# Performance work log

Measured on AMD Instinct MI355X. Metric: run time of the kernel, lower is better.

The kernel has to match this reference:

```python
import jax, jax.numpy as jnp
import numpy as np
import math

D = 2048            # fc_feat_size (hardcoded sqrt(2048) scale in source)
IMAGES = 20         # images_per_person
NEIGHBOR = 5        # neighbor_size (sliding window width)
T = IMAGES - NEIGHBOR + 1   # number of windows = 16
SCALE = 1.0 / math.sqrt(2048.0)


def _attention(x, Wq, bq, Wk, bk, Wv, bv):
    # x: [N, L, D] -> [N, L, D]; bmm-softmax-bmm as in source
    q = x @ Wq.T + bq
    k = x @ Wk.T + bk
    v = x @ Wv.T + bv
    dot = jnp.einsum('nld,nmd->nlm', q, k) * SCALE
    w = jax.nn.softmax(dot, axis=-1)
    return jnp.einsum('nlm,nmd->nld', w, v)


def _lstm_final(x, Wih, Whh, bih, bhh):
    # PyTorch-convention LSTM (gates i,f,g,o); x: [N, L, D] -> final hidden [N, H]
    N = x.shape[0]
    H = Whh.shape[1]
    xg = x @ Wih.T + (bih + bhh)   # [N, L, 4H] precompute input projections

    def step(carry, xt):
        h, c = carry
        gates = xt + h @ Whh.T
        i, f, g, o = jnp.split(gates, 4, axis=-1)
        c = jax.nn.sigmoid(f) * c + jax.nn.sigmoid(i) * jnp.tanh(g)
        h = jax.nn.sigmoid(o) * jnp.tanh(c)
        return (h, c), None

    init = (jnp.zeros((N, H), x.dtype), jnp.zeros((N, H), x.dtype))
    (h, _), _ = jax.lax.scan(step, init, jnp.swapaxes(xg, 0, 1))
    return h


def _layernorm(x, g, b, eps=1e-5):
    mu = jnp.mean(x, axis=-1, keepdims=True)
    var = jnp.var(x, axis=-1, keepdims=True)
    return (x - mu) * jax.lax.rsqrt(var + eps) * g + b


def setup_inputs() -> dict:
    key = jax.random.key(0)
    ks = iter(jax.random.split(key, 32))
    s = 0.02
    p = {}
    p['fc_feats'] = jax.random.normal(next(ks), (64, IMAGES, D), jnp.float32)
    for pre in ('nsa', 'sa'):
        for nm in ('Wq', 'Wk', 'Wv'):
            p[f'{pre}_{nm}'] = jax.random.normal(next(ks), (D, D), jnp.float32) * s
        for nm in ('bq', 'bk', 'bv'):
            p[f'{pre}_{nm}'] = jnp.zeros((D,), jnp.float32)
        p[f'{pre}_Wih'] = jax.random.normal(next(ks), (4 * D, D), jnp.float32) * s
        p[f'{pre}_Whh'] = jax.random.normal(next(ks), (4 * D, D), jnp.float32) * s
        p[f'{pre}_bih'] = jnp.zeros((4 * D,), jnp.float32)
        p[f'{pre}_bhh'] = jnp.zeros((4 * D,), jnp.float32)
    p['ln_g'] = jnp.ones((D,), jnp.float32)
    p['ln_b'] = jnp.zeros((D,), jnp.float32)
    return p


def reference(fc_feats,
              nsa_Wq, nsa_Wk, nsa_Wv, nsa_bq, nsa_bk, nsa_bv,
              nsa_Wih, nsa_Whh, nsa_bih, nsa_bhh,
              sa_Wq, sa_Wk, sa_Wv, sa_bq, sa_bk, sa_bv,
              sa_Wih, sa_Whh, sa_bih, sa_bhh,
              ln_g, ln_b):
    B = fc_feats.shape[0]
    # Sliding windows: window t covers images [t, t+NEIGHBOR) -> [B, T, W, D]
    idx = jnp.arange(T)[:, None] + jnp.arange(NEIGHBOR)[None, :]
    windows = fc_feats[:, idx]                       # [B, T, W, D]
    wflat = windows.reshape(B * T, NEIGHBOR, D)
    # NeighboringSelfAttention: attention within window + LSTM final state
    att = _attention(wflat, nsa_Wq, nsa_bq, nsa_Wk, nsa_bk, nsa_Wv, nsa_bv)
    nsa = _lstm_final(att, nsa_Wih, nsa_Whh, nsa_bih, nsa_bhh)  # [B*T, D]
    nsa_feats = nsa.reshape(B, T, D)
    new_nsa_feats = _layernorm(nsa_feats, ln_g, ln_b)
    # SelfAttention over the T window summaries + LSTM final state
    att2 = _attention(new_nsa_feats, sa_Wq, sa_bq, sa_Wk, sa_bk, sa_Wv, sa_bv)
    sa_feats = _lstm_final(att2, sa_Wih, sa_Whh, sa_bih, sa_bhh)  # [B, D]
    return (sa_feats, new_nsa_feats)
```

## Files before the change

### kernel.cpp

```cpp
#include <hip/hip_runtime.h>
#include <hip/hip_bf16.h>

typedef unsigned int  u32;
typedef unsigned short u16;

typedef __bf16 bf16x8 __attribute__((ext_vector_type(8)));
typedef float  f32x4  __attribute__((ext_vector_type(4)));

#define D2048 2048
#define SCALE 0.022097086912079612f

__device__ __forceinline__ u32 f2bfbits(float f) {
    u32 u = __float_as_uint(f);
    return (u + 0x7FFFu + ((u >> 16) & 1u)) >> 16;
}
__device__ __forceinline__ u32 pack2(float a, float b) {
    return f2bfbits(a) | (f2bfbits(b) << 16);
}
__device__ __forceinline__ float bf2f(u32 h) {
    return __uint_as_float(h << 16);
}
__device__ __forceinline__ void unpack8(uint4 v, float* f) {
    f[0] = bf2f(v.x & 0xFFFFu); f[1] = bf2f(v.x >> 16);
    f[2] = bf2f(v.y & 0xFFFFu); f[3] = bf2f(v.y >> 16);
    f[4] = bf2f(v.z & 0xFFFFu); f[5] = bf2f(v.z >> 16);
    f[6] = bf2f(v.w & 0xFFFFu); f[7] = bf2f(v.w >> 16);
}
__device__ __forceinline__ float sigmf(float x) { return 1.f / (1.f + __expf(-x)); }
__device__ __forceinline__ float tanhf_(float x) {
    x = fminf(15.f, fmaxf(-15.f, x));
    float e = __expf(2.f * x);
    return (e - 1.f) / (e + 1.f);
}

__device__ __forceinline__ void gload_lds16(const u16* g, u16* l) {
    __builtin_amdgcn_global_load_lds(
        (const __attribute__((address_space(1))) unsigned int*)g,
        (__attribute__((address_space(3))) unsigned int*)l,
        16, 0, 0);
}

struct CvtArgs {
    const float* src[8];
    u16*         dst[8];
    int          n4[8];
    int          nseg;
};
__global__ __launch_bounds__(256) void cvt_multi(CvtArgs a) {
    int stride = gridDim.x * 256;
    for (int s = 0; s < a.nseg; ++s) {
        const float4* S = reinterpret_cast<const float4*>(a.src[s]);
        uint2*        D = reinterpret_cast<uint2*>(a.dst[s]);
        int n4 = a.n4[s];
        for (int i = blockIdx.x * 256 + threadIdx.x; i < n4; i += stride) {
            float4 v = S[i];
            uint2 p;
            p.x = pack2(v.x, v.y);
            p.y = pack2(v.z, v.w);
            D[i] = p;
        }
    }
}

template <bool OUT_BF16>
__global__ __launch_bounds__(512, 2) void gemm256(const u16* __restrict__ A, int lda,
                                                  const u16* __restrict__ B,
                                                  void* __restrict__ C0,
                                                  int M, int N, int K) {
    __shared__ u16 Ab[2][16384];
    __shared__ u16 Bb[2][16384];

    const int tid  = threadIdx.x;
    const int lane = tid & 63;
    const int wid  = tid >> 6;
    const int wm   = wid >> 2;
    const int wn   = wid & 3;
    const int l15  = lane & 15, l4 = lane >> 4;
    const int rowBase = blockIdx.y * 256;
    const int colBase = blockIdx.x * 256;

    const int srow8 = lane >> 3;
    const int scw   = ((lane & 7) ^ srow8) * 8;
    const u16* gA = A + (size_t)(rowBase + wid * 8 + srow8) * lda + scw;
    const u16* gB = B + (size_t)(colBase + wid * 8 + srow8) * (size_t)K + scw;
    const int ldsW = wid * 512;

#define STAGE_A(buf, koff, q) \
    gload_lds16(gA + (size_t)((q) * 64) * lda + (koff), &Ab[buf][(q) * 4096 + ldsW])
#define STAGE_B(buf, koff, q) \
    gload_lds16(gB + (size_t)((q) * 64) * (size_t)K + (koff), &Bb[buf][(q) * 4096 + ldsW])

    f32x4 acc[8][4];
#pragma unroll
    for (int m = 0; m < 8; m++)
#pragma unroll
        for (int n = 0; n < 4; n++) acc[m][n] = f32x4{0.f, 0.f, 0.f, 0.f};

    const int nt = K >> 6;

#pragma unroll
    for (int q = 0; q < 4; ++q) { STAGE_A(0, 0, q); STAGE_B(0, 0, q); }

    const int swzA = (l15 & 7);

    for (int t = 0; t < nt; ++t) {
        const int cur = t & 1;
        const int nxt = cur ^ 1;
        const int kN  = (t + 1) << 6;
        const bool more = (t + 1 < nt);

        if (more) {
            STAGE_A(nxt, kN, 0);
            STAGE_A(nxt, kN, 1);
            asm volatile("s_waitcnt vmcnt(2)" ::: "memory");
        } else {
            asm volatile("s_waitcnt vmcnt(0)" ::: "memory");
        }
        __builtin_amdgcn_s_barrier();

        bf16x8 bfrag[4][2];
#pragma unroll
        for (int n = 0; n < 4; ++n)
#pragma unroll
            for (int kk = 0; kk < 2; ++kk)
                bfrag[n][kk] = *reinterpret_cast<const bf16x8*>(
                    &Bb[cur][(wn * 64 + n * 16 + l15) * 64 +
                             (((kk * 4 + l4) ^ swzA) * 8)]);

#pragma unroll
        for (int p = 0; p < 4; ++p) {
            bf16x8 afr[2][2];
#pragma unroll
            for (int mi = 0; mi < 2; ++mi)
#pragma unroll
                for (int kk = 0; kk < 2; ++kk)
                    afr[mi][kk] = *reinterpret_cast<const bf16x8*>(
                        &Ab[cur][(wm * 128 + (p * 2 + mi) * 16 + l15) * 64 +
                                 (((kk * 4 + l4) ^ swzA) * 8)]);
            if (more) {
                if (p == 0)      { STAGE_A(nxt, kN, 2); STAGE_A(nxt, kN, 3); }
                else if (p == 1) { STAGE_B(nxt, kN, 0); STAGE_B(nxt, kN, 1); }
                else if (p == 2) { STAGE_B(nxt, kN, 2); STAGE_B(nxt, kN, 3); }
            }
            __builtin_amdgcn_s_barrier();
            __builtin_amdgcn_sched_barrier(0);
            __builtin_amdgcn_s_setprio(1);
#pragma unroll
            for (int kk = 0; kk < 2; ++kk)
#pragma unroll
                for (int mi = 0; mi < 2; ++mi)
#pragma unroll
                    for (int n = 0; n < 4; ++n)
                        acc[p * 2 + mi][n] = __builtin_amdgcn_mfma_f32_16x16x32_bf16(
                            afr[mi][kk], bfrag[n][kk], acc[p * 2 + mi][n], 0, 0, 0);
            __builtin_amdgcn_s_setprio(0);
            __builtin_amdgcn_sched_barrier(0);
            __builtin_amdgcn_s_barrier();
        }
    }
#undef STAGE_A
#undef STAGE_B

#pragma unroll
    for (int m = 0; m < 8; ++m) {
        int row0 = rowBase + wm * 128 + m * 16 + l4 * 4;
#pragma unroll
        for (int n = 0; n < 4; ++n) {
            int col = colBase + wn * 64 + n * 16 + l15;
#pragma unroll
            for (int rr = 0; rr < 4; ++rr) {
                if (OUT_BF16)
                    ((u16*)C0)[(size_t)(row0 + rr) * N + col] = (u16)f2bfbits(acc[m][n][rr]);
                else
                    ((float*)C0)[(size_t)(row0 + rr) * N + col] = acc[m][n][rr];
            }
        }
    }
}

__global__ __launch_bounds__(256) void gemm_qkv(const u16* __restrict__ A,
                                                const u16* __restrict__ B0,
                                                const u16* __restrict__ B1,
                                                const u16* __restrict__ B2,
                                                const float* __restrict__ bias0,
                                                const float* __restrict__ bias1,
                                                const float* __restrict__ bias2,
                                                u16* __restrict__ Cout,
                                                size_t zCstride,
                                                int M, int N, int K) {
    __shared__ u16 Abuf[2][128 * 64];
    __shared__ u16 Bbuf[2][128 * 64];

    const int tid  = threadIdx.x;
    const int lane = tid & 63;
    const int wave = tid >> 6;
    const int wr   = (wave >> 1) * 64;
    const int wc   = (wave & 1) * 64;
    const int rowBase = blockIdx.y * 128;
    const int colBase = blockIdx.x * 128;
    const int l15 = lane & 15, l4 = lane >> 4;
    const int srow = lane >> 3;
    const int scol = (lane & 7) * 8;

    const int z = blockIdx.z;
    const u16* B      = (z == 0) ? B0 : ((z == 1) ? B1 : B2);
    const float* bias = (z == 0) ? bias0 : ((z == 1) ? bias1 : bias2);
    u16* C = Cout + (size_t)z * zCstride;

    const u16* ga = A + (size_t)(rowBase + wave * 32 + srow) * K + scol;
    const u16* gb = B + (size_t)(colBase + wave * 32 + srow) * K + scol;
    const int ldsOff = (wave * 32) * 64;

    f32x4 acc[4][4];
#pragma unroll
    for (int i = 0; i < 4; i++)
#pragma unroll
        for (int j = 0; j < 4; j++) acc[i][j] = f32x4{0.f, 0.f, 0.f, 0.f};

    const int nt = K >> 6;

#pragma unroll
    for (int i = 0; i < 4; ++i) {
        gload_lds16(ga + (size_t)(i * 8) * K, &Abuf[0][ldsOff + i * 8 * 64]);
        gload_lds16(gb + (size_t)(i * 8) * K, &Bbuf[0][ldsOff + i * 8 * 64]);
    }

    for (int t = 0; t < nt; ++t) {
        const int cur = t & 1;
        if (t + 1 < nt) {
            const int k1 = (t + 1) << 6;
#pragma unroll
            for (int i = 0; i < 4; ++i) {
                gload_lds16(ga + (size_t)(i * 8) * K + k1,
                            &Abuf[cur ^ 1][ldsOff + i * 8 * 64]);
                gload_lds16(gb + (size_t)(i * 8) * K + k1,
                            &Bbuf[cur ^ 1][ldsOff + i * 8 * 64]);
            }
            asm volatile("s_waitcnt vmcnt(8)" ::: "memory");
        } else {
            asm volatile("s_waitcnt vmcnt(0)" ::: "memory");
        }
        __builtin_amdgcn_s_barrier();
        __builtin_amdgcn_sched_barrier(0);
#pragma unroll
        for (int kk = 0; kk < 2; ++kk) {
            bf16x8 af[4], bfr[4];
#pragma unroll
            for (int i = 0; i < 4; i++) {
                af[i]  = *reinterpret_cast<const bf16x8*>(
                    &Abuf[cur][(wr + i * 16 + l15) * 64 + kk * 32 + l4 * 8]);
                bfr[i] = *reinterpret_cast<const bf16x8*>(
                    &Bbuf[cur][(wc + i * 16 + l15) * 64 + kk * 32 + l4 * 8]);
            }
#pragma unroll
            for (int i = 0; i < 4; i++)
#pragma unroll
                for (int j = 0; j < 4; j++)
                    acc[i][j] = __builtin_amdgcn_mfma_f32_16x16x32_bf16(af[i], bfr[j],
                                                                        acc[i][j], 0, 0, 0);
        }
        __builtin_amdgcn_sched_barrier(0);
        __builtin_amdgcn_s_barrier();
    }

#pragma unroll
    for (int i = 0; i < 4; i++) {
        int row0 = rowBase + wr + i * 16 + l4 * 4;
#pragma unroll
        for (int j = 0; j < 4; j++) {
            int col = colBase + wc + j * 16 + l15;
            float bv = bias[col];
#pragma unroll
            for (int rr = 0; rr < 4; rr++)
                C[(size_t)(row0 + rr) * N + col] = (u16)f2bfbits(acc[i][j][rr] + bv);
        }
    }
}

__global__ __launch_bounds__(256) void gemm128_bf(const u16* __restrict__ A,
                                                  const u16* __restrict__ B,
                                                  u16* __restrict__ C,
                                                  int M, int N, int K) {
    __shared__ u16 Abuf[2][128 * 64];
    __shared__ u16 Bbuf[2][128 * 64];

    const int tid  = threadIdx.x;
    const int lane = tid & 63;
    const int wave = tid >> 6;
    const int wr   = (wave >> 1) * 64;
    const int wc   = (wave & 1) * 64;
    const int rowBase = blockIdx.y * 128;
    const int colBase = blockIdx.x * 128;
    const int l15 = lane & 15, l4 = lane >> 4;
    const int srow = lane >> 3;
    const int scol = (lane & 7) * 8;

    const u16* ga = A + (size_t)(rowBase + wave * 32 + srow) * K + scol;
    const u16* gb = B + (size_t)(colBase + wave * 32 + srow) * K + scol;
    const int ldsOff = (wave * 32) * 64;

    f32x4 acc[4][4];
#pragma unroll
    for (int i = 0; i < 4; i++)
#pragma unroll
        for (int j = 0; j < 4; j++) acc[i][j] = f32x4{0.f, 0.f, 0.f, 0.f};

    const int nt = K >> 6;

#pragma unroll
    for (int i = 0; i < 4; ++i) {
        gload_lds16(ga + (size_t)(i * 8) * K, &Abuf[0][ldsOff + i * 8 * 64]);
        gload_lds16(gb + (size_t)(i * 8) * K, &Bbuf[0][ldsOff + i * 8 * 64]);
    }

    for (int t = 0; t < nt; ++t) {
        const int cur = t & 1;
        if (t + 1 < nt) {
            const int k1 = (t + 1) << 6;
#pragma unroll
            for (int i = 0; i < 4; ++i) {
                gload_lds16(ga + (size_t)(i * 8) * K + k1,
                            &Abuf[cur ^ 1][ldsOff + i * 8 * 64]);
                gload_lds16(gb + (size_t)(i * 8) * K + k1,
                            &Bbuf[cur ^ 1][ldsOff + i * 8 * 64]);
            }
            asm volatile("s_waitcnt vmcnt(8)" ::: "memory");
        } else {
            asm volatile("s_waitcnt vmcnt(0)" ::: "memory");
        }
        __builtin_amdgcn_s_barrier();
        __builtin_amdgcn_sched_barrier(0);
#pragma unroll
        for (int kk = 0; kk < 2; ++kk) {
            bf16x8 af[4], bfr[4];
#pragma unroll
            for (int i = 0; i < 4; i++) {
                af[i]  = *reinterpret_cast<const bf16x8*>(
                    &Abuf[cur][(wr + i * 16 + l15) * 64 + kk * 32 + l4 * 8]);
                bfr[i] = *reinterpret_cast<const bf16x8*>(
                    &Bbuf[cur][(wc + i * 16 + l15) * 64 + kk * 32 + l4 * 8]);
            }
#pragma unroll
            for (int i = 0; i < 4; i++)
#pragma unroll
                for (int j = 0; j < 4; j++)
                    acc[i][j] = __builtin_amdgcn_mfma_f32_16x16x32_bf16(af[i], bfr[j],
                                                                        acc[i][j], 0, 0, 0);
        }
        __builtin_amdgcn_sched_barrier(0);
        __builtin_amdgcn_s_barrier();
    }

#pragma unroll
    for (int i = 0; i < 4; i++) {
        int row0 = rowBase + wr + i * 16 + l4 * 4;
#pragma unroll
        for (int j = 0; j < 4; j++) {
            int col = colBase + wc + j * 16 + l15;
#pragma unroll
            for (int rr = 0; rr < 4; rr++)
                C[(size_t)(row0 + rr) * N + col] = (u16)f2bfbits(acc[i][j][rr]);
        }
    }
}

template <bool LAST>
__global__ __launch_bounds__(256) void gemm_gate128(
    const u16* __restrict__ A,
    const u16* __restrict__ B,
    const u16* __restrict__ xg,
    int xg_stride,
    const float* __restrict__ bih,
    const float* __restrict__ bhh,
    float* __restrict__ c,
    u16* __restrict__ hbf_out,
    float* __restrict__ hf,
    int K) {
    __shared__ u16 smem[32768];
    u16* Ab = smem;
    u16* Bb = smem + 16384;

    const int tid = threadIdx.x, lane = tid & 63, wave = tid >> 6;
    const int wr = (wave >> 1) * 64, wc = (wave & 1) * 64;
    const int l15 = lane & 15, l4 = lane >> 4;
    const int srow = lane >> 3, scol = (lane & 7) * 8;
    const int jBase = blockIdx.x * 32;
    const int rowBase = blockIdx.y * 128;

    const u16* ga = A + (size_t)(rowBase + wave * 32 + srow) * K + scol;
    const u16* gb[4];
#pragma unroll
    for (int i = 0; i < 4; ++i) {
        int lc = wave * 32 + i * 8 + srow;
        int br = jBase + (lc & 31) + (lc >> 5) * 2048;
        gb[i] = B + (size_t)br * K + scol;
    }
    const int ldsOff = (wave * 32) * 64;

    f32x4 acc[4][4];
#pragma unroll
    for (int i = 0; i < 4; i++)
#pragma unroll
        for (int j = 0; j < 4; j++) acc[i][j] = f32x4{0.f, 0.f, 0.f, 0.f};

    const int nt = K >> 6;
#pragma unroll
    for (int i = 0; i < 4; ++i) {
        gload_lds16(ga + (size_t)(i * 8) * K, &Ab[ldsOff + i * 8 * 64]);
        gload_lds16(gb[i], &Bb[ldsOff + i * 8 * 64]);
    }

    for (int t = 0; t < nt; ++t) {
        const int cur = (t & 1) * 8192;
        if (t + 1 < nt) {
            const int k1 = (t + 1) << 6;
            const int nxt = ((t + 1) & 1) * 8192;
#pragma unroll
            for (int i = 0; i < 4; ++i) {
                gload_lds16(ga + (size_t)(i * 8) * K + k1, &Ab[nxt + ldsOff + i * 8 * 64]);
                gload_lds16(gb[i] + k1, &Bb[nxt + ldsOff + i * 8 * 64]);
            }
            asm volatile("s_waitcnt vmcnt(8)" ::: "memory");
        } else {
            asm volatile("s_waitcnt vmcnt(0)" ::: "memory");
        }
        __builtin_amdgcn_s_barrier();
        __builtin_amdgcn_sched_barrier(0);
#pragma unroll
        for (int kk = 0; kk < 2; ++kk) {
            bf16x8 af[4], bfr[4];
#pragma unroll
            for (int i = 0; i < 4; i++) {
                af[i]  = *reinterpret_cast<const bf16x8*>(
                    &Ab[cur + (wr + i * 16 + l15) * 64 + kk * 32 + l4 * 8]);
                bfr[i] = *reinterpret_cast<const bf16x8*>(
                    &Bb[cur + (wc + i * 16 + l15) * 64 + kk * 32 + l4 * 8]);
            }
#pragma unroll
            for (int i = 0; i < 4; i++)
#pragma unroll
                for (int j = 0; j < 4; j++)
                    acc[i][j] = __builtin_amdgcn_mfma_f32_16x16x32_bf16(af[i], bfr[j],
                                                                        acc[i][j], 0, 0, 0);
        }
        __builtin_amdgcn_sched_barrier(0);
        __builtin_amdgcn_s_barrier();
    }

    float* Cs = (float*)smem;
#pragma unroll
    for (int i = 0; i < 4; i++)
#pragma unroll
        for (int j = 0; j < 4; j++)
#pragma unroll
            for (int rr = 0; rr < 4; rr++)
                Cs[(wr + i * 16 + l4 * 4 + rr) * 128 + (wc + j * 16 + l15)] =
                    acc[i][j][rr];
    __syncthreads();

    const int j  = tid & 31;
    const int rb = tid >> 5;
    const int gj = jBase + j;
    const float bi_ = bih[gj]        + bhh[gj];
    const float bf_ = bih[gj + 2048] + bhh[gj + 2048];
    const float bg_ = bih[gj + 4096] + bhh[gj + 4096];
    const float bo_ = bih[gj + 6144] + bhh[gj + 6144];
#pragma unroll
    for (int k = 0; k < 16; ++k) {
        int r = rb * 16 + k;
        int n = rowBase + r;
        const u16* xr = xg + (size_t)n * xg_stride;
        float gi = Cs[r * 128 + j]      + bf2f((u32)xr[gj])        + bi_;
        float gf = Cs[r * 128 + 32 + j] + bf2f((u32)xr[gj + 2048]) + bf_;
        float gg = Cs[r * 128 + 64 + j] + bf2f((u32)xr[gj + 4096]) + bg_;
        float go = Cs[r * 128 + 96 + j] + bf2f((u32)xr[gj + 6144]) + bo_;
        size_t idx = (size_t)n * 2048 + gj;
        float cc = c[idx];
        float cn = sigmf(gf) * cc + sigmf(gi) * tanhf_(gg);
        float hn = sigmf(go) * tanhf_(cn);
        c[idx] = cn;
        hbf_out[idx] = (u16)f2bfbits(hn);
        if (LAST) hf[idx] = hn;
    }
}

__global__ __launch_bounds__(256) void gemm_gate64v2(
    const u16* __restrict__ A,
    const u16* __restrict__ B,
    const u16* __restrict__ xg,
    int xg_stride,
    const float* __restrict__ bih,
    const float* __restrict__ bhh,
    float* __restrict__ c,
    u16* __restrict__ hbf_out,
    float* __restrict__ hf,
    int K) {
    __shared__ u16 smem[12288];
    u16* Ab = smem;
    u16* Bb = smem + 8192;

    const int tid = threadIdx.x, lane = tid & 63, wave = tid >> 6;
    const int l15 = lane & 15, l4 = lane >> 4;
    const int srow = lane >> 3, scol = (lane & 7) * 8;
    const int jb = blockIdx.x;

    const u16* ga = A + (size_t)(wave * 16 + srow) * K + scol;
    const u16* gb = B + (size_t)(jb * 8 + srow + wave * 2048) * K + scol;
    const int aOff = (wave * 16) * 64;
    const int bOff = (wave * 8) * 64;

    f32x4 acc0 = f32x4{0.f, 0.f, 0.f, 0.f};
    f32x4 acc1 = f32x4{0.f, 0.f, 0.f, 0.f};

    const int nt = K >> 6;
    gload_lds16(ga,                 &Ab[aOff]);
    gload_lds16(ga + (size_t)8 * K, &Ab[aOff + 512]);
    gload_lds16(gb,                 &Bb[bOff]);

    for (int t = 0; t < nt; ++t) {
        const int curA = (t & 1) * 4096;
        const int curB = (t & 1) * 2048;
        if (t + 1 < nt) {
            const int k1 = (t + 1) << 6;
            const int nxA = ((t + 1) & 1) * 4096;
            const int nxB = ((t + 1) & 1) * 2048;
            gload_lds16(ga + k1,                 &Ab[nxA + aOff]);
            gload_lds16(ga + (size_t)8 * K + k1, &Ab[nxA + aOff + 512]);
            gload_lds16(gb + k1,                 &Bb[nxB + bOff]);
            asm volatile("s_waitcnt vmcnt(3)" ::: "memory");
        } else {
            asm volatile("s_waitcnt vmcnt(0)" ::: "memory");
        }
        __builtin_amdgcn_s_barrier();
        __builtin_amdgcn_sched_barrier(0);
#pragma unroll
        for (int kk = 0; kk < 2; ++kk) {
            bf16x8 af = *reinterpret_cast<const bf16x8*>(
                &Ab[curA + (wave * 16 + l15) * 64 + kk * 32 + l4 * 8]);
            bf16x8 b0 = *reinterpret_cast<const bf16x8*>(
                &Bb[curB + (l15) * 64 + kk * 32 + l4 * 8]);
            bf16x8 b1 = *reinterpret_cast<const bf16x8*>(
                &Bb[curB + (16 + l15) * 64 + kk * 32 + l4 * 8]);
            acc0 = __builtin_amdgcn_mfma_f32_16x16x32_bf16(af, b0, acc0, 0, 0, 0);
            acc1 = __builtin_amdgcn_mfma_f32_16x16x32_bf16(af, b1, acc1, 0, 0, 0);
        }
        __builtin_amdgcn_sched_barrier(0);
        __builtin_amdgcn_s_barrier();
    }

    float* Cs = (float*)smem;
    {
        int row0 = wave * 16 + l4 * 4;
#pragma unroll
        for (int rr = 0; rr < 4; ++rr) {
            Cs[(row0 + rr) * 32 + l15]      = acc0[rr];
            Cs[(row0 + rr) * 32 + 16 + l15] = acc1[rr];
        }
    }
    __syncthreads();

    const int j  = tid & 7;
    const int gj = jb * 8 + j;
    const float bi_ = bih[gj]        + bhh[gj];
    const float bf_ = bih[gj + 2048] + bhh[gj + 2048];
    const float bg_ = bih[gj + 4096] + bhh[gj + 4096];
    const float bo_ = bih[gj + 6144] + bhh[gj + 6144];
#pragma unroll
    for (int k = 0; k < 2; ++k) {
        int row = (tid >> 3) + k * 32;
        const u16* xr = xg + (size_t)row * xg_stride;
        float gi = Cs[row * 32 + j]      + bf2f((u32)xr[gj])        + bi_;
        float gf = Cs[row * 32 + 8 + j]  + bf2f((u32)xr[gj + 2048]) + bf_;
        float gg = Cs[row * 32 + 16 + j] + bf2f((u32)xr[gj + 4096]) + bg_;
        float go = Cs[row * 32 + 24 + j] + bf2f((u32)xr[gj + 6144]) + bo_;
        size_t idx = (size_t)row * 2048 + gj;
        float cc = c[idx];
        float cn = sigmf(gf) * cc + sigmf(gi) * tanhf_(gg);
        float hn = sigmf(go) * tanhf_(cn);
        c[idx] = cn;
        hbf_out[idx] = (u16)f2bfbits(hn);
        if (hf) hf[idx] = hn;
    }
}

__global__ __launch_bounds__(256) void lstm_gate0(const u16* __restrict__ xg,
                                                  int xg_stride,
                                                  const float* __restrict__ bih,
                                                  const float* __restrict__ bhh,
                                                  float* __restrict__ c,
                                                  u16* __restrict__ hbf,
                                                  int rows) {
    int idx = blockIdx.x * 256 + threadIdx.x;
    int total = rows * 512;
    if (idx >= total) return;
    int n  = idx >> 9;
    int j4 = (idx & 511) * 4;

    const u16* xr = xg + (size_t)n * xg_stride + j4;
    float4 gi, gg, go;
    {
        uint2 ri = *reinterpret_cast<const uint2*>(xr);
        uint2 rg = *reinterpret_cast<const uint2*>(xr + 4096);
        uint2 ro = *reinterpret_cast<const uint2*>(xr + 6144);
        gi = {bf2f(ri.x & 0xFFFFu), bf2f(ri.x >> 16), bf2f(ri.y & 0xFFFFu), bf2f(ri.y >> 16)};
        gg = {bf2f(rg.x & 0xFFFFu), bf2f(rg.x >> 16), bf2f(rg.y & 0xFFFFu), bf2f(rg.y >> 16)};
        go = {bf2f(ro.x & 0xFFFFu), bf2f(ro.x >> 16), bf2f(ro.y & 0xFFFFu), bf2f(ro.y >> 16)};
    }
    float4 bi1 = *reinterpret_cast<const float4*>(bih + j4);
    float4 bg1 = *reinterpret_cast<const float4*>(bih + 4096 + j4);
    float4 bo1 = *reinterpret_cast<const float4*>(bih + 6144 + j4);
    float4 bi2 = *reinterpret_cast<const float4*>(bhh + j4);
    float4 bg2 = *reinterpret_cast<const float4*>(bhh + 4096 + j4);
    float4 bo2 = *reinterpret_cast<const float4*>(bhh + 6144 + j4);

    gi.x += bi1.x + bi2.x; gi.y += bi1.y + bi2.y; gi.z += bi1.z + bi2.z; gi.w += bi1.w + bi2.w;
    gg.x += bg1.x + bg2.x; gg.y += bg1.y + bg2.y; gg.z += bg1.z + bg2.z; gg.w += bg1.w + bg2.w;
    go.x += bo1.x + bo2.x; go.y += bo1.y + bo2.y; go.z += bo1.z + bo2.z; go.w += bo1.w + bo2.w;

    float cx = sigmf(gi.x) * tanhf_(gg.x);
    float cy = sigmf(gi.y) * tanhf_(gg.y);
    float cz = sigmf(gi.z) * tanhf_(gg.z);
    float cw = sigmf(gi.w) * tanhf_(gg.w);
    float hx = sigmf(go.x) * tanhf_(cx);
    float hy = sigmf(go.y) * tanhf_(cy);
    float hz = sigmf(go.z) * tanhf_(cz);
    float hw_ = sigmf(go.w) * tanhf_(cw);

    float4 co = {cx, cy, cz, cw};
    *reinterpret_cast<float4*>(c + (size_t)n * 2048 + j4) = co;
    uint2 hp;
    hp.x = pack2(hx, hy);
    hp.y = pack2(hz, hw_);
    *reinterpret_cast<uint2*>(hbf + (size_t)n * 2048 + j4) = hp;
}

__global__ __launch_bounds__(256) void attn_win5(const u16* __restrict__ q0,
                                                 const u16* __restrict__ k0,
                                                 const u16* __restrict__ v0,
                                                 u16* __restrict__ att) {
    int n = blockIdx.x;
    int b = n >> 4, t = n & 15;
    int tid = threadIdx.x, lane = tid & 63, wave = tid >> 6;
    int d0 = tid * 8;
    size_t base = (size_t)(b * 20 + t) * D2048;

    float qv[5][8];
#pragma unroll
    for (int i = 0; i < 5; i++) {
        uint4 v = *reinterpret_cast<const uint4*>(q0 + base + (size_t)i * D2048 + d0);
        unpack8(v, qv[i]);
    }
    float part[25];
#pragma unroll
    for (int p = 0; p < 25; p++) part[p] = 0.f;
#pragma unroll
    for (int m = 0; m < 5; m++) {
        float kv[8];
        uint4 v = *reinterpret_cast<const uint4*>(k0 + base + (size_t)m * D2048 + d0);
        unpack8(v, kv);
#pragma unroll
        for (int l = 0; l < 5; l++)
#pragma unroll
            for (int j = 0; j < 8; j++) part[l * 5 + m] += qv[l][j] * kv[j];
    }
#pragma unroll
    for (int p = 0; p < 25; p++) {
        float s = part[p];
#pragma unroll
        for (int msk = 32; msk; msk >>= 1) s += __shfl_xor(s, msk, 64);
        part[p] = s;
    }
    __shared__ float wred[4][25];
    __shared__ float wmat[25];
    if (lane == 0) {
#pragma unroll
        for (int p = 0; p < 25; p++) wred[wave][p] = part[p];
    }
    __syncthreads();
    if (tid < 5) {
        int l = tid;
        float dv[5], mx = -1e30f;
#pragma unroll
        for (int m = 0; m < 5; m++) {
            dv[m] = (wred[0][l * 5 + m] + wred[1][l * 5 + m] + wred[2][l * 5 + m] +
                     wred[3][l * 5 + m]) * SCALE;
            mx = fmaxf(mx, dv[m]);
        }
        float ssum = 0.f;
#pragma unroll
        for (int m = 0; m < 5; m++) { dv[m] = __expf(dv[m] - mx); ssum += dv[m]; }
        float inv = 1.f / ssum;
#pragma unroll
        for (int m = 0; m < 5; m++) wmat[l * 5 + m] = dv[m] * inv;
    }
    __syncthreads();

    float oacc[5][8];
#pragma unroll
    for (int l = 0; l < 5; l++)
#pragma unroll
        for (int j = 0; j < 8; j++) oacc[l][j] = 0.f;
#pragma unroll
    for (int m = 0; m < 5; m++) {
        float vv[8];
        uint4 v = *reinterpret_cast<const uint4*>(v0 + base + (size_t)m * D2048 + d0);
        unpack8(v, vv);
#pragma unroll
        for (int l = 0; l < 5; l++) {
            float w = wmat[l * 5 + m];
#pragma unroll
            for (int j = 0; j < 8; j++) oacc[l][j] += w * vv[j];
        }
    }
#pragma unroll
    for (int l = 0; l < 5; l++) {
        uint4 p;
        p.x = pack2(oacc[l][0], oacc[l][1]);
        p.y = pack2(oacc[l][2], oacc[l][3]);
        p.z = pack2(oacc[l][4], oacc[l][5]);
        p.w = pack2(oacc[l][6], oacc[l][7]);
        *reinterpret_cast<uint4*>(att + (size_t)(n * 5 + l) * D2048 + d0) = p;
    }
}

__global__ __launch_bounds__(256) void attn_seq16(const u16* __restrict__ q2,
                                                  const u16* __restrict__ k2,
                                                  const u16* __restrict__ v2,
                                                  u16* __restrict__ att2) {
    int r = blockIdx.x;
    int b = r >> 4;
    int tid = threadIdx.x, lane = tid & 63, wave = tid >> 6;
    int d0 = tid * 8;
    size_t kbase = (size_t)b * 16 * D2048;

    float qv[8];
    {
        uint4 v = *reinterpret_cast<const uint4*>(q2 + (size_t)r * D2048 + d0);
        unpack8(v, qv);
    }
    float part[16];
#pragma unroll
    for (int m = 0; m < 16; m++) part[m] = 0.f;
#pragma unroll
    for (int m = 0; m < 16; m++) {
        float kv[8];
        uint4 v = *reinterpret_cast<const uint4*>(k2 + kbase + (size_t)m * D2048 + d0);
        unpack8(v, kv);
#pragma unroll
        for (int j = 0; j < 8; j++) part[m] += qv[j] * kv[j];
    }
#pragma unroll
    for (int m = 0; m < 16; m++) {
        float s = part[m];
#pragma unroll
        for (int msk = 32; msk; msk >>= 1) s += __shfl_xor(s, msk, 64);
        part[m] = s;
    }
    __shared__ float wred[4][16];
    __shared__ float wmat[16];
    if (lane == 0) {
#pragma unroll
        for (int m = 0; m < 16; m++) wred[wave][m] = part[m];
    }
    __syncthreads();
    if (tid == 0) {
        float dv[16], mx = -1e30f;
#pragma unroll
        for (int m = 0; m < 16; m++) {
            dv[m] = (wred[0][m] + wred[1][m] + wred[2][m] + wred[3][m]) * SCALE;
            mx = fmaxf(mx, dv[m]);
        }
        float ssum = 0.f;
#pragma unroll
        for (int m = 0; m < 16; m++) { dv[m] = __expf(dv[m] - mx); ssum += dv[m]; }
        float inv = 1.f / ssum;
#pragma unroll
        for (int m = 0; m < 16; m++) wmat[m] = dv[m] * inv;
    }
    __syncthreads();

    float oacc[8];
#pragma unroll
    for (int j = 0; j < 8; j++) oacc[j] = 0.f;
#pragma unroll
    for (int m = 0; m < 16; m++) {
        float vv[8];
        uint4 v = *reinterpret_cast<const uint4*>(v2 + kbase + (size_t)m * D2048 + d0);
        unpack8(v, vv);
        float w = wmat[m];
#pragma unroll
        for (int j = 0; j < 8; j++) oacc[j] += w * vv[j];
    }
    uint4 p;
    p.x = pack2(oacc[0], oacc[1]);
    p.y = pack2(oacc[2], oacc[3]);
    p.z = pack2(oacc[4], oacc[5]);
    p.w = pack2(oacc[6], oacc[7]);
    *reinterpret_cast<uint4*>(att2 + (size_t)r * D2048 + d0) = p;
}

__global__ __launch_bounds__(256) void layernorm_k(const float* __restrict__ x,
                                                   const float* __restrict__ g,
                                                   const float* __restrict__ b,
                                                   float* __restrict__ y,
                                                   u16* __restrict__ ybf) {
    int row = blockIdx.x;
    int tid = threadIdx.x, lane = tid & 63, wave = tid >> 6;
    const float* xr = x + (size_t)row * D2048;
    int j = tid * 8;
    float4 v1 = *reinterpret_cast<const float4*>(xr + j);
    float4 v2 = *reinterpret_cast<const float4*>(xr + j + 4);
    float s  = v1.x + v1.y + v1.z + v1.w + v2.x + v2.y + v2.z + v2.w;
    float s2 = v1.x * v1.x + v1.y * v1.y + v1.z * v1.z + v1.w * v1.w +
               v2.x * v2.x + v2.y * v2.y + v2.z * v2.z + v2.w * v2.w;
#pragma unroll
    for (int msk = 32; msk; msk >>= 1) {
        s  += __shfl_xor(s, msk, 64);
        s2 += __shfl_xor(s2, msk, 64);
    }
    __shared__ float red[4][2];
    if (lane == 0) { red[wave][0] = s; red[wave][1] = s2; }
    __syncthreads();
    s  = red[0][0] + red[1][0] + red[2][0] + red[3][0];
    s2 = red[0][1] + red[1][1] + red[2][1] + red[3][1];
    float mu  = s * (1.f / 2048.f);
    float var = s2 * (1.f / 2048.f) - mu * mu;
    float rs  = __frsqrt_rn(var + 1e-5f);

    float4 g1 = *reinterpret_cast<const float4*>(g + j);
    float4 g2 = *reinterpret_cast<const float4*>(g + j + 4);
    float4 b1 = *reinterpret_cast<const float4*>(b + j);
    float4 b2 = *reinterpret_cast<const float4*>(b + j + 4);
    float o[8];
    o[0] = (v1.x - mu) * rs * g1.x + b1.x;
    o[1] = (v1.y - mu) * rs * g1.y + b1.y;
    o[2] = (v1.z - mu) * rs * g1.z + b1.z;
    o[3] = (v1.w - mu) * rs * g1.w + b1.w;
    o[4] = (v2.x - mu) * rs * g2.x + b2.x;
    o[5] = (v2.y - mu) * rs * g2.y + b2.y;
    o[6] = (v2.z - mu) * rs * g2.z + b2.z;
    o[7] = (v2.w - mu) * rs * g2.w + b2.w;
    float4 o1 = {o[0], o[1], o[2], o[3]};
    float4 o2 = {o[4], o[5], o[6], o[7]};
    float* yr = y + (size_t)row * D2048;
    *reinterpret_cast<float4*>(yr + j)     = o1;
    *reinterpret_cast<float4*>(yr + j + 4) = o2;
    uint4 p;
    p.x = pack2(o[0], o[1]);
    p.y = pack2(o[2], o[3]);
    p.z = pack2(o[4], o[5]);
    p.w = pack2(o[6], o[7]);
    *reinterpret_cast<uint4*>(ybf + (size_t)row * D2048 + j) = p;
}

static inline void launch_qkv(hipStream_t s, const u16* A, const u16* Wq,
                              const u16* Wk, const u16* Wv, const float* bq,
                              const float* bk, const float* bv, u16* out,
                              int M, int N, int K) {
    dim3 grid(N / 128, M / 128, 3);
    gemm_qkv<<<grid, 256, 0, s>>>(A, Wq, Wk, Wv, bq, bk, bv, out,
                                  (size_t)M * N, M, N, K);
}

extern "C" void kernel_launch(void* const* d_in, const int* in_sizes, int n_in,
                              void* d_out, int out_size, void* d_ws, size_t ws_size,
                              hipStream_t stream) {
    const float* fc      = (const float*)d_in[0];
    const float* nsa_Wq  = (const float*)d_in[1];
    const float* nsa_Wk  = (const float*)d_in[2];
    const float* nsa_Wv  = (const float*)d_in[3];
    const float* nsa_bq  = (const float*)d_in[4];
    const float* nsa_bk  = (const float*)d_in[5];
    const float* nsa_bv  = (const float*)d_in[6];
    const float* nsa_Wih = (const float*)d_in[7];
    const float* nsa_Whh = (const float*)d_in[8];
    const float* nsa_bih = (const float*)d_in[9];
    const float* nsa_bhh = (const float*)d_in[10];
    const float* sa_Wq   = (const float*)d_in[11];
    const float* sa_Wk   = (const float*)d_in[12];
    const float* sa_Wv   = (const float*)d_in[13];
    const float* sa_bq   = (const float*)d_in[14];
    const float* sa_bk   = (const float*)d_in[15];
    const float* sa_bv   = (const float*)d_in[16];
    const float* sa_Wih  = (const float*)d_in[17];
    const float* sa_Whh  = (const float*)d_in[18];
    const float* sa_bih  = (const float*)d_in[19];
    const float* sa_bhh  = (const float*)d_in[20];
    const float* ln_g    = (const float*)d_in[21];
    const float* ln_b    = (const float*)d_in[22];

    float* outF   = (float*)d_out;
    float* out_sa = outF;
    float* out_ln = outF + 131072;

    char* W = (char*)d_ws;
    u16* W_q   = (u16*)(W + 0);
    u16* W_k   = (u16*)(W + 8388608);
    u16* W_v   = (u16*)(W + 16777216);
    u16* W_ih  = (u16*)(W + 25165824);
    u16* W_hh1 = (u16*)(W + 58720256);
    u16* W_hh2 = (u16*)(W + 92274688);
    u16*   Xbf  = (u16*)(W + 125829120);
    u16*   q0   = (u16*)(W + 131072000);
    u16*   att1 = (u16*)(W + 146800640);
    u16*   xg   = (u16*)(W + 167772160);
    float* h1    = (float*)(W + 0);
    float* c1    = (float*)(W + 8388608);
    u16*   hbfA  = (u16*)(W + 16777216);
    u16*   hbfB  = (u16*)(W + 131072000);
    u16*   lnbf  = Xbf;
    u16*   q2    = q0;
    u16*   att2  = att1;
    float* c2    = (float*)(W + 148373504);
    u16*   h2bfA = (u16*)(W + 148897792);
    u16*   h2bfB = (u16*)(W + 149422080);

    {
        CvtArgs a{};
        a.src[0] = fc;      a.dst[0] = Xbf;   a.n4[0] = 655360;
        a.src[1] = nsa_Wq;  a.dst[1] = W_q;   a.n4[1] = 1048576;
        a.src[2] = nsa_Wk;  a.dst[2] = W_k;   a.n4[2] = 1048576;
        a.src[3] = nsa_Wv;  a.dst[3] = W_v;   a.n4[3] = 1048576;
        a.src[4] = nsa_Wih; a.dst[4] = W_ih;  a.n4[4] = 4194304;
        a.src[5] = nsa_Whh; a.dst[5] = W_hh1; a.n4[5] = 4194304;
        a.src[6] = sa_Whh;  a.dst[6] = W_hh2; a.n4[6] = 4194304;
        a.nseg = 7;
        cvt_multi<<<2048, 256, 0, stream>>>(a);
    }

    launch_qkv(stream, Xbf, W_q, W_k, W_v, nsa_bq, nsa_bk, nsa_bv, q0, 1280, 2048, 2048);

    attn_win5<<<1024, 256, 0, stream>>>(q0, q0 + 2621440, q0 + 5242880, att1);

    gemm256<true><<<dim3(32, 20), 512, 0, stream>>>(att1, 2048, W_ih, xg,
                                                    5120, 8192, 2048);

    lstm_gate0<<<2048, 256, 0, stream>>>(xg, 40960, nsa_bih, nsa_bhh, c1, hbfA, 1024);
    {
        u16* hin = hbfA;
        for (int t = 1; t < 5; ++t) {
            u16* hout = (t & 1) ? hbfB : hbfA;
            if (t == 4)
                gemm_gate128<true><<<dim3(64, 8), 256, 0, stream>>>(
                    hin, W_hh1, xg + (size_t)t * 8192, 40960, nsa_bih, nsa_bhh,
                    c1, hout, h1, 2048);
            else
                gemm_gate128<false><<<dim3(64, 8), 256, 0, stream>>>(
                    hin, W_hh1, xg + (size_t)t * 8192, 40960, nsa_bih, nsa_bhh,
                    c1, hout, nullptr, 2048);
            hin = hout;
        }
    }

    layernorm_k<<<1024, 256, 0, stream>>>(h1, ln_g, ln_b, out_ln, lnbf);

    {
        CvtArgs a{};
        a.src[0] = sa_Wq;  a.dst[0] = W_q;  a.n4[0] = 1048576;
        a.src[1] = sa_Wk;  a.dst[1] = W_k;  a.n4[1] = 1048576;
        a.src[2] = sa_Wv;  a.dst[2] = W_v;  a.n4[2] = 1048576;
        a.src[3] = sa_Wih; a.dst[3] = W_ih; a.n4[3] = 4194304;
        a.nseg = 4;
        cvt_multi<<<2048, 256, 0, stream>>>(a);
    }

    launch_qkv(stream, lnbf, W_q, W_k, W_v, sa_bq, sa_bk, sa_bv, q2, 1024, 2048, 2048);

    attn_seq16<<<1024, 256, 0, stream>>>(q2, q2 + 2097152, q2 + 4194304, att2);

    gemm128_bf<<<dim3(64, 8), 256, 0, stream>>>(att2, W_ih, xg, 1024, 8192, 2048);

    lstm_gate0<<<128, 256, 0, stream>>>(xg, 131072, sa_bih, sa_bhh, c2, h2bfA, 64);
    {
        u16* hin = h2bfA;
        for (int t = 1; t < 16; ++t) {
            u16* hout = (t & 1) ? h2bfB : h2bfA;
            gemm_gate64v2<<<dim3(256), 256, 0, stream>>>(
                hin, W_hh2, xg + (size_t)t * 8192, 131072, sa_bih, sa_bhh,
                c2, hout, (t == 15) ? out_sa : nullptr, 2048);
            hin = hout;
        }
    }
}
```

Measured before the change: 953.7 us.

## Fuse SA LSTM recurrence into one persistent cooperative kernel with grid sync

Replaces the initial gate kernel and the 15 per-timestep GEMM+gate launches of the second LSTM with a single cooperative kernel. The kernel computes step 0 inline, then loops over timesteps, separating them with a threadfence and a grid-wide sync. This removes 15 kernel launches and their inter-kernel gaps. In exchange it adds grid barrier costs, and it requires all 256 blocks to be co-resident on the device.

```diff
diff --git a/kernel.cpp b/kernel.cpp
--- a/kernel.cpp
+++ b/kernel.cpp
@@ -1,5 +1,8 @@
 #include <hip/hip_runtime.h>
 #include <hip/hip_bf16.h>
+#include <hip/hip_cooperative_groups.h>
+
+namespace cg = cooperative_groups;
 
 typedef unsigned int  u32;
 typedef unsigned short u16;
@@ -484,17 +487,16 @@
     }
 }
 
-__global__ __launch_bounds__(256) void gemm_gate64v2(
-    const u16* __restrict__ A,
-    const u16* __restrict__ B,
+__global__ __launch_bounds__(256) void sa_lstm_persist(
+    const u16* __restrict__ Whh,
     const u16* __restrict__ xg,
-    int xg_stride,
     const float* __restrict__ bih,
     const float* __restrict__ bhh,
     float* __restrict__ c,
-    u16* __restrict__ hbf_out,
-    float* __restrict__ hf,
-    int K) {
+    u16* __restrict__ hA,
+    u16* __restrict__ hB,
+    float* __restrict__ out_sa) {
+    cg::grid_group gridg = cg::this_grid();
     __shared__ u16 smem[12288];
     u16* Ab = smem;
     u16* Bb = smem + 8192;
@@ -503,61 +505,8 @@
     const int l15 = lane & 15, l4 = lane >> 4;
     const int srow = lane >> 3, scol = (lane & 7) * 8;
     const int jb = blockIdx.x;
-
-    const u16* ga = A + (size_t)(wave * 16 + srow) * K + scol;
-    const u16* gb = B + (size_t)(jb * 8 + srow + wave * 2048) * K + scol;
-    const int aOff = (wave * 16) * 64;
-    const int bOff = (wave * 8) * 64;
-
-    f32x4 acc0 = f32x4{0.f, 0.f, 0.f, 0.f};
-    f32x4 acc1 = f32x4{0.f, 0.f, 0.f, 0.f};
-
+    const int K = 2048;
     const int nt = K >> 6;
-    gload_lds16(ga,                 &Ab[aOff]);
-    gload_lds16(ga + (size_t)8 * K, &Ab[aOff + 512]);
-    gload_lds16(gb,                 &Bb[bOff]);
-
-    for (int t = 0; t < nt; ++t) {
-        const int curA = (t & 1) * 4096;
-        const int curB = (t & 1) * 2048;
-        if (t + 1 < nt) {
-            const int k1 = (t + 1) << 6;
-            const int nxA = ((t + 1) & 1) * 4096;
-            const int nxB = ((t + 1) & 1) * 2048;
-            gload_lds16(ga + k1,                 &Ab[nxA + aOff]);
-            gload_lds16(ga + (size_t)8 * K + k1, &Ab[nxA + aOff + 512]);
-            gload_lds16(gb + k1,                 &Bb[nxB + bOff]);
-            asm volatile("s_waitcnt vmcnt(3)" ::: "memory");
-        } else {
-            asm volatile("s_waitcnt vmcnt(0)" ::: "memory");
-        }
-        __builtin_amdgcn_s_barrier();
-        __builtin_amdgcn_sched_barrier(0);
-#pragma unroll
-        for (int kk = 0; kk < 2; ++kk) {
-            bf16x8 af = *reinterpret_cast<const bf16x8*>(
-                &Ab[curA + (wave * 16 + l15) * 64 + kk * 32 + l4 * 8]);
-            bf16x8 b0 = *reinterpret_cast<const bf16x8*>(
-                &Bb[curB + (l15) * 64 + kk * 32 + l4 * 8]);
-            bf16x8 b1 = *reinterpret_cast<const bf16x8*>(
-                &Bb[curB + (16 + l15) * 64 + kk * 32 + l4 * 8]);
-            acc0 = __builtin_amdgcn_mfma_f32_16x16x32_bf16(af, b0, acc0, 0, 0, 0);
-            acc1 = __builtin_amdgcn_mfma_f32_16x16x32_bf16(af, b1, acc1, 0, 0, 0);
-        }
-        __builtin_amdgcn_sched_barrier(0);
-        __builtin_amdgcn_s_barrier();
-    }
-
-    float* Cs = (float*)smem;
-    {
-        int row0 = wave * 16 + l4 * 4;
-#pragma unroll
-        for (int rr = 0; rr < 4; ++rr) {
-            Cs[(row0 + rr) * 32 + l15]      = acc0[rr];
-            Cs[(row0 + rr) * 32 + 16 + l15] = acc1[rr];
-        }
-    }
-    __syncthreads();
 
     const int j  = tid & 7;
     const int gj = jb * 8 + j;
@@ -565,21 +514,99 @@
     const float bf_ = bih[gj + 2048] + bhh[gj + 2048];
     const float bg_ = bih[gj + 4096] + bhh[gj + 4096];
     const float bo_ = bih[gj + 6144] + bhh[gj + 6144];
+
 #pragma unroll
     for (int k = 0; k < 2; ++k) {
         int row = (tid >> 3) + k * 32;
-        const u16* xr = xg + (size_t)row * xg_stride;
-        float gi = Cs[row * 32 + j]      + bf2f((u32)xr[gj])        + bi_;
-        float gf = Cs[row * 32 + 8 + j]  + bf2f((u32)xr[gj + 2048]) + bf_;
-        float gg = Cs[row * 32 + 16 + j] + bf2f((u32)xr[gj + 4096]) + bg_;
-        float go = Cs[row * 32 + 24 + j] + bf2f((u32)xr[gj + 6144]) + bo_;
-        size_t idx = (size_t)row * 2048 + gj;
-        float cc = c[idx];
-        float cn = sigmf(gf) * cc + sigmf(gi) * tanhf_(gg);
+        const u16* xr = xg + (size_t)row * 131072;
+        float gi = bf2f((u32)xr[gj])        + bi_;
+        float gg = bf2f((u32)xr[gj + 4096]) + bg_;
+        float go = bf2f((u32)xr[gj + 6144]) + bo_;
+        float cn = sigmf(gi) * tanhf_(gg);
         float hn = sigmf(go) * tanhf_(cn);
-        c[idx] = cn;
-        hbf_out[idx] = (u16)f2bfbits(hn);
-        if (hf) hf[idx] = hn;
+        c[(size_t)row * 2048 + gj]  = cn;
+        hA[(size_t)row * 2048 + gj] = (u16)f2bfbits(hn);
+    }
+    __threadfence();
+    gridg.sync();
+
+    const u16* gb = Whh + (size_t)(jb * 8 + srow + wave * 2048) * K + scol;
+    const int aOff = (wave * 16) * 64;
+    const int bOff = (wave * 8) * 64;
+
+    for (int t = 1; t < 16; ++t) {
+        const u16* A = (t & 1) ? hA : hB;
+        u16* hout    = (t & 1) ? hB : hA;
+        const u16* ga = A + (size_t)(wave * 16 + srow) * K + scol;
+
+        f32x4 acc0 = f32x4{0.f, 0.f, 0.f, 0.f};
+        f32x4 acc1 = f32x4{0.f, 0.f, 0.f, 0.f};
+        gload_lds16(ga,                 &Ab[aOff]);
+        gload_lds16(ga + (size_t)8 * K, &Ab[aOff + 512]);
+        gload_lds16(gb,                 &Bb[bOff]);
+
+        for (int tt = 0; tt < nt; ++tt) {
+            const int curA = (tt & 1) * 4096;
+            const int curB = (tt & 1) * 2048;
+            if (tt + 1 < nt) {
+                const int k1 = (tt + 1) << 6;
+                const int nxA = ((tt + 1) & 1) * 4096;
+                const int nxB = ((tt + 1) & 1) * 2048;
+                gload_lds16(ga + k1,                 &Ab[nxA + aOff]);
+                gload_lds16(ga + (size_t)8 * K + k1, &Ab[nxA + aOff + 512]);
+                gload_lds16(gb + k1,                 &Bb[nxB + bOff]);
+                asm volatile("s_waitcnt vmcnt(3)" ::: "memory");
+            } else {
+                asm volatile("s_waitcnt vmcnt(0)" ::: "memory");
+            }
+            __builtin_amdgcn_s_barrier();
+            __builtin_amdgcn_sched_barrier(0);
+#pragma unroll
+            for (int kk = 0; kk < 2; ++kk) {
+                bf16x8 af = *reinterpret_cast<const bf16x8*>(
+                    &Ab[curA + (wave * 16 + l15) * 64 + kk * 32 + l4 * 8]);
+                bf16x8 b0 = *reinterpret_cast<const bf16x8*>(
+                    &Bb[curB + (l15) * 64 + kk * 32 + l4 * 8]);
+                bf16x8 b1 = *reinterpret_cast<const bf16x8*>(
+                    &Bb[curB + (16 + l15) * 64 + kk * 32 + l4 * 8]);
+                acc0 = __builtin_amdgcn_mfma_f32_16x16x32_bf16(af, b0, acc0, 0, 0, 0);
+                acc1 = __builtin_amdgcn_mfma_f32_16x16x32_bf16(af, b1, acc1, 0, 0, 0);
+            }
+            __builtin_amdgcn_sched_barrier(0);
+            __builtin_amdgcn_s_barrier();
+        }
+
+        float* Cs = (float*)smem;
+        {
+            int row0 = wave * 16 + l4 * 4;
+#pragma unroll
+            for (int rr = 0; rr < 4; ++rr) {
+                Cs[(row0 + rr) * 32 + l15]      = acc0[rr];
+                Cs[(row0 + rr) * 32 + 16 + l15] = acc1[rr];
+            }
+        }
+        __syncthreads();
+
+#pragma unroll
+        for (int k = 0; k < 2; ++k) {
+            int row = (tid >> 3) + k * 32;
+            const u16* xr = xg + (size_t)row * 131072 + (size_t)t * 8192;
+            float gi = Cs[row * 32 + j]      + bf2f((u32)xr[gj])        + bi_;
+            float gf = Cs[row * 32 + 8 + j]  + bf2f((u32)xr[gj + 2048]) + bf_;
+            float gg = Cs[row * 32 + 16 + j] + bf2f((u32)xr[gj + 4096]) + bg_;
+            float go = Cs[row * 32 + 24 + j] + bf2f((u32)xr[gj + 6144]) + bo_;
+            size_t idx = (size_t)row * 2048 + gj;
+            float cc = c[idx];
+            float cn = sigmf(gf) * cc + sigmf(gi) * tanhf_(gg);
+            float hn = sigmf(go) * tanhf_(cn);
+            c[idx] = cn;
+            hout[idx] = (u16)f2bfbits(hn);
+            if (t == 15) out_sa[idx] = hn;
+        }
+        if (t < 15) {
+            __threadfence();
+            gridg.sync();
+        }
     }
 }
 
@@ -970,15 +997,10 @@
 
     gemm128_bf<<<dim3(64, 8), 256, 0, stream>>>(att2, W_ih, xg, 1024, 8192, 2048);
 
-    lstm_gate0<<<128, 256, 0, stream>>>(xg, 131072, sa_bih, sa_bhh, c2, h2bfA, 64);
     {
-        u16* hin = h2bfA;
-        for (int t = 1; t < 16; ++t) {
-            u16* hout = (t & 1) ? h2bfB : h2bfA;
-            gemm_gate64v2<<<dim3(256), 256, 0, stream>>>(
-                hin, W_hh2, xg + (size_t)t * 8192, 131072, sa_bih, sa_bhh,
-                c2, hout, (t == 15) ? out_sa : nullptr, 2048);
-            hin = hout;
-        }
-    }
-}
+        void* ka[] = {(void*)&W_hh2, (void*)&xg, (void*)&sa_bih, (void*)&sa_bhh,
+                      (void*)&c2, (void*)&h2bfA, (void*)&h2bfB, (void*)&out_sa};
+        hipLaunchCooperativeKernel(sa_lstm_persist, dim3(256), dim3(256),
+                                   ka, 0, stream);
+    }
+}
```

Measured after the change: 1.820 ms. 90.8% more time.
